# Kernel optimization log

Measured on AMD Instinct MI355X. Metric: run time of the kernel, lower is better.

## Reference

```python
import jax, jax.numpy as jnp
import numpy as np

B, T, N, F, NH, K = 512, 32, 64, 32, 4, 4
D = N * F          # model_dim = 2048
GH = N             # GRU hidden = num_channels
EPS_BN = 1e-5
EPS_LN = 1e-5


def _normalize_A(A):
    # relu -> zero diag -> symmetrize -> sym-normalized Laplacian -> rescale (lmax=2)
    n = A.shape[-1]
    eye = jnp.eye(n, dtype=A.dtype)
    A = jax.nn.relu(A) * (1.0 - eye)
    A = A + A.T
    dinv = 1.0 / jnp.sqrt(jnp.sum(A, axis=1) + 1e-10)
    L = eye - dinv[:, None] * A * dinv[None, :]
    return 2.0 * L / 2.0 - eye


def _cheby(L, k):
    # Chebyshev polynomial basis T_0..T_{k-1} of L, stacked [k, N, N]
    n = L.shape[-1]
    sup = [jnp.eye(n, dtype=L.dtype), L]
    for _ in range(2, k):
        sup.append(2.0 * L @ sup[-1] - sup[-2])
    return jnp.stack(sup[:k])


def _bn(x, g, b, axes):
    # training-mode batch norm (biased variance), stats over `axes`
    m = jnp.mean(x, axes, keepdims=True)
    v = jnp.mean((x - m) ** 2, axes, keepdims=True)
    return (x - m) / jnp.sqrt(v + EPS_BN) * g + b


def _forward(x, A, cheb_W, bn1_g, bn1_b, bn2_g, bn2_b,
             Wq, Wk, Wv, Wf, bf, ln_g, ln_b,
             W_ih, W_hh, b_ih, b_hh, lin_W, lin_b, cls_W, cls_b):
    Bsz, Tn, Nn, Fn = x.shape
    xt = jnp.swapaxes(x, 0, 1)                                   # [T,B,N,F]
    # DGCNN BN1: stats over (B, N) per feature, per time step
    xb = _bn(xt, bn1_g[:, None, None, :], bn1_b[:, None, None, :], (1, 2))
    # per-timestep normalized Laplacian and Chebyshev basis
    Ls = jax.vmap(_normalize_A)(A)                               # [T,N,N]
    cheb = jax.vmap(lambda L: _cheby(L, K))(Ls)                  # [T,K,N,N]
    # Chebynet: sum_k (T_k(L) @ x) @ W_k, then relu
    res = jnp.einsum('tknm,tbmf,tkfo->tbno', cheb, xb, cheb_W)   # [T,B,N,F]
    res = jax.nn.relu(res)
    # per-timestep BatchNorm over flattened (B*N, F)
    y = res.reshape(Tn, Bsz * Nn, Fn)
    y = _bn(y, bn2_g[:, None, :], bn2_b[:, None, :], (1,))
    y = jax.nn.sigmoid(y)                                        # [T,B*N,F]
    # replicate torch's stack/transpose/reshape exactly
    y_seq = jnp.swapaxes(y, 0, 1).reshape(Bsz, Tn, Nn * Fn)      # [B,T,D]
    # multi-head attention (no bias on q/k/v, scale = dh^-0.5)
    dh = D // NH
    def heads(z, W):
        return jnp.swapaxes((z @ W).reshape(Bsz, Tn, NH, dh), 1, 2)  # [B,H,T,dh]
    q, k, v = heads(y_seq, Wq), heads(y_seq, Wk), heads(y_seq, Wv)
    attn = jax.nn.softmax(jnp.einsum('bhqd,bhkd->bhqk', q, k) * dh ** -0.5, axis=-1)
    ctx = jnp.einsum('bhqk,bhkd->bhqd', attn, v)
    ctx = jnp.swapaxes(ctx, 1, 2).reshape(Bsz, Tn, D)
    out = ctx @ Wf + bf
    h = y_seq + out
    mu = jnp.mean(h, -1, keepdims=True)
    var = jnp.mean((h - mu) ** 2, -1, keepdims=True)
    h = (h - mu) / jnp.sqrt(var + EPS_LN) * ln_g + ln_b          # [B,T,D]
    # GRU (torch gate convention), scan over time
    def step(hprev, xt_):
        gi = xt_ @ W_ih.T + b_ih                                  # [B,3H]
        gh = hprev @ W_hh.T + b_hh
        ir, iz, inn = jnp.split(gi, 3, axis=-1)
        hr, hz, hn = jnp.split(gh, 3, axis=-1)
        r = jax.nn.sigmoid(ir + hr)
        zg = jax.nn.sigmoid(iz + hz)
        ng = jnp.tanh(inn + r * hn)
        hnew = (1.0 - zg) * ng + zg * hprev
        return hnew, hnew
    h0 = jnp.zeros((Bsz, GH), x.dtype)
    _, hs = jax.lax.scan(step, h0, jnp.swapaxes(h, 0, 1))        # [T,B,GH]
    y_gru = jax.nn.sigmoid(jnp.swapaxes(hs, 0, 1))               # [B,T,GH]
    out_flat = y_gru.reshape(Bsz, Tn * GH)
    proj = jax.nn.sigmoid(out_flat @ lin_W.T + lin_b)
    proj = proj / jnp.maximum(jnp.linalg.norm(proj, axis=-1, keepdims=True), 1e-12)
    y_pred = jax.nn.sigmoid(out_flat @ cls_W.T + cls_b)
    return proj[:, None, :], y_pred


def setup_inputs() -> dict:
    key = jax.random.key(0)
    ks = jax.random.split(key, 12)
    def nrm(k, shape, s):
        return jax.random.normal(k, shape, dtype=jnp.float32) * s
    return {
        'x': jax.random.normal(ks[0], (B, T, N, F), dtype=jnp.float32),
        'A': jax.random.uniform(ks[1], (T, N, N), minval=0.01, maxval=0.5, dtype=jnp.float32),
        'cheb_W': nrm(ks[2], (T, K, F, F), 0.1),
        'bn1_g': jnp.ones((T, F), jnp.float32), 'bn1_b': jnp.zeros((T, F), jnp.float32),
        'bn2_g': jnp.ones((T, F), jnp.float32), 'bn2_b': jnp.zeros((T, F), jnp.float32),
        'Wq': nrm(ks[3], (D, D), 0.02), 'Wk': nrm(ks[4], (D, D), 0.02), 'Wv': nrm(ks[5], (D, D), 0.02),
        'Wf': nrm(ks[6], (D, D), 0.02), 'bf': jnp.zeros((D,), jnp.float32),
        'ln_g': jnp.ones((D,), jnp.float32), 'ln_b': jnp.zeros((D,), jnp.float32),
        'W_ih': nrm(ks[7], (3 * GH, D), 0.02), 'W_hh': nrm(ks[8], (3 * GH, GH), 0.1),
        'b_ih': jnp.zeros((3 * GH,), jnp.float32), 'b_hh': jnp.zeros((3 * GH,), jnp.float32),
        'lin_W': nrm(ks[9], (128, T * GH), 0.05), 'lin_b': jnp.zeros((128,), jnp.float32),
        'cls_W': nrm(ks[10], (3, T * GH), 0.05), 'cls_b': jnp.zeros((3,), jnp.float32),
    }


def reference(x, A, cheb_W, bn1_g, bn1_b, bn2_g, bn2_b,
              Wq, Wk, Wv, Wf, bf, ln_g, ln_b,
              W_ih, W_hh, b_ih, b_hh, lin_W, lin_b, cls_W, cls_b):
    return _forward(x, A, cheb_W, bn1_g, bn1_b, bn2_g, bn2_b,
                    Wq, Wk, Wv, Wf, bf, ln_g, ln_b,
                    W_ih, W_hh, b_ih, b_hh, lin_W, lin_b, cls_W, cls_b)
```

## Files before the change

kernel.cpp:

```cpp
#include <hip/hip_runtime.h>
#include <hip/hip_bf16.h>

typedef unsigned short u16;
typedef __attribute__((ext_vector_type(8))) short short8;
typedef __attribute__((ext_vector_type(4))) short short4_;
typedef __attribute__((ext_vector_type(4))) float f32x4;

__device__ __forceinline__ u16 f2bf(float f){
  union { float fv; unsigned int u; } v; v.fv = f;
  unsigned int u = v.u;
  u = u + 0x7FFFu + ((u >> 16) & 1u);
  return (u16)(u >> 16);
}
__device__ __forceinline__ float bf2f(u16 h){
  union { unsigned int u; float fv; } v; v.u = ((unsigned int)h) << 16; return v.fv;
}
__device__ __forceinline__ float sigmoidf_(float x){ return 1.f/(1.f + __expf(-x)); }
__device__ __forceinline__ float tanhf_(float x){ return 2.f/(1.f + __expf(-2.f*x)) - 1.f; }

__device__ __forceinline__ void gload16(const void* g, void* l){
  __builtin_amdgcn_global_load_lds(
      (const __attribute__((address_space(1))) void*)g,
      (__attribute__((address_space(3))) void*)l, 16, 0, 0);
}
__device__ __forceinline__ f32x4 mfma_bf16(short8 a, short8 b, f32x4 c){
  return __builtin_amdgcn_mfma_f32_16x16x32_bf16(a, b, c, 0, 0, 0);
}

#define ASM_VMCNT2 asm volatile("s_waitcnt vmcnt(2)" ::: "memory")
#define ASM_VMCNT0 asm volatile("s_waitcnt vmcnt(0)" ::: "memory")
#define ASM_LGK0   asm volatile("s_waitcnt lgkmcnt(0)" ::: "memory")
#define SCHB       __builtin_amdgcn_sched_barrier(0)
#define SBAR       do { asm volatile("" ::: "memory"); __builtin_amdgcn_s_barrier(); asm volatile("" ::: "memory"); } while(0)

constexpr size_t OFF_A    = 0;
constexpr size_t OFF_B    = 67108864;
constexpr size_t OFF_C    = OFF_B + 67108864;
constexpr size_t OFF_D    = OFF_C + 201326592;
constexpr size_t OFF_E    = OFF_D + 67108864;
constexpr size_t OFF_WFT  = OFF_E + 25165824;
constexpr size_t OFF_WIH  = OFF_WFT + 8388608;
constexpr size_t OFF_LHAT = OFF_WIH + 1048576;
constexpr size_t OFF_B1P  = OFF_LHAT + 524288;
constexpr size_t OFF_B1S  = OFF_B1P + 524288;
constexpr size_t OFF_B2P  = OFF_B1S + 8192;
constexpr size_t OFF_B2S  = OFF_B2P + 4194304;
constexpr size_t OFF_TC   = OFF_LHAT;
constexpr size_t OFF_WT2  = OFF_C;
constexpr size_t OFF_GI   = OFF_C;
constexpr size_t OFF_OUTF = OFF_C + 16777216;

__global__ __launch_bounds__(256) void wtrans_kernel(const float* __restrict__ Wq, const float* __restrict__ Wk,
                                                     const float* __restrict__ Wv, const float* __restrict__ Wf,
                                                     u16* __restrict__ WqkvT, u16* __restrict__ WfT)
{
  const int k0 = blockIdx.x*64, n0 = blockIdx.y*64, z = blockIdx.z;
  const float* src = (z==0)?Wq:(z==1)?Wk:(z==2)?Wv:Wf;
  u16* dst = (z<3) ? (WqkvT + (size_t)z*2048*2048) : WfT;
  __shared__ float tile[64][65];
  const int c = threadIdx.x & 63, r0 = threadIdx.x >> 6;
#pragma unroll
  for (int i=0;i<16;++i){ int r = r0 + i*4; tile[r][c] = src[(size_t)(k0+r)*2048 + n0 + c]; }
  __syncthreads();
#pragma unroll
  for (int i=0;i<16;++i){ int r = r0 + i*4; dst[(size_t)(n0+r)*2048 + k0 + c] = f2bf(tile[c][r]); }
}

__global__ __launch_bounds__(256) void wih_kernel(const float* __restrict__ Wih, u16* __restrict__ WT)
{
  const int row = blockIdx.x, tid = threadIdx.x;
#pragma unroll
  for (int i=0;i<8;++i){ int col = tid + i*256;
    float v = (row < 192) ? Wih[(size_t)row*2048 + col] : 0.f;
    WT[(size_t)row*2048 + col] = f2bf(v);
  }
}

__global__ __launch_bounds__(256) void bn1_part_kernel(const float* __restrict__ x, float* __restrict__ part)
{
  const int t = blockIdx.x, sl = blockIdx.y;
  const int f = threadIdx.x & 31, grp = threadIdx.x >> 5;
  float s = 0.f, ss = 0.f;
  for (int bb = 0; bb < 8; ++bb){
    const int b = sl*8 + bb;
    const float* xp = x + ((size_t)(b*32 + t))*2048;
    for (int i = 0; i < 8; ++i){
      int n = i*8 + grp;
      float v = xp[n*32 + f];
      s += v; ss += v*v;
    }
  }
  __shared__ float red[8][32][2];
  red[grp][f][0] = s; red[grp][f][1] = ss;
  __syncthreads();
  if (threadIdx.x < 32){
    float S=0, SS=0;
    for (int g=0; g<8; ++g){ S += red[g][threadIdx.x][0]; SS += red[g][threadIdx.x][1]; }
    size_t o = (((size_t)t*64 + sl)*32 + threadIdx.x)*2;
    part[o] = S; part[o+1] = SS;
  }
}

__global__ __launch_bounds__(256) void bn1_fin_kernel(const float* __restrict__ part, const float* __restrict__ g1,
                                                      const float* __restrict__ b1, float* __restrict__ out)
{
  const int t = blockIdx.x;
  const int f = threadIdx.x & 31, grp = threadIdx.x >> 5;
  float s=0, ss=0;
  for (int sl = grp; sl < 64; sl += 8){
    size_t o = (((size_t)t*64 + sl)*32 + f)*2;
    s += part[o]; ss += part[o+1];
  }
  __shared__ float red[8][32][2];
  red[grp][f][0]=s; red[grp][f][1]=ss;
  __syncthreads();
  if (threadIdx.x < 32){
    float S=0, SS=0;
    for (int g=0; g<8; ++g){ S+=red[g][threadIdx.x][0]; SS+=red[g][threadIdx.x][1]; }
    float mean = S*(1.f/32768.f);
    float var  = SS*(1.f/32768.f) - mean*mean;
    float sc   = g1[t*32+threadIdx.x]*rsqrtf(var + 1e-5f);
    out[(t*32+threadIdx.x)*2]   = sc;
    out[(t*32+threadIdx.x)*2+1] = b1[t*32+threadIdx.x] - mean*sc;
  }
}

__global__ __launch_bounds__(256) void lap2_kernel(const float* __restrict__ A, const float* __restrict__ chebW,
                                                   u16* __restrict__ Tcat, u16* __restrict__ WTg)
{
  const int t = blockIdx.x, tid = threadIdx.x;
  __shared__ float Ar[64][68];
  __shared__ float L1[64][68];
  __shared__ float T2s[64][68];
  __shared__ float dr[64];
#pragma unroll
  for (int i=0;i<16;++i){ int idx = tid + i*256; int r = idx>>6, c = idx&63;
    float v = A[(size_t)t*4096 + idx]; v = fmaxf(v, 0.f); if (r==c) v = 0.f;
    Ar[r][c] = v; }
  __syncthreads();
  if (tid < 64){
    float s = 0;
    for (int c2=0;c2<64;++c2) s += Ar[tid][c2] + Ar[c2][tid];
    dr[tid] = rsqrtf(s + 1e-10f);
  }
  __syncthreads();
#pragma unroll
  for (int i=0;i<16;++i){ int idx = tid + i*256; int r = idx>>6, c = idx&63;
    L1[r][c] = -(Ar[r][c] + Ar[c][r]) * dr[r] * dr[c];
  }
  __syncthreads();
  const int row = tid >> 2, c0 = (tid & 3) << 4;
  float a2[16];
#pragma unroll
  for (int j=0;j<16;++j) a2[j] = 0.f;
#pragma unroll 4
  for (int m=0;m<64;++m){
    float lv = L1[row][m];
#pragma unroll
    for (int j=0;j<16;++j) a2[j] += lv*L1[m][c0+j];
  }
#pragma unroll
  for (int j=0;j<16;++j) T2s[row][c0+j] = 2.f*a2[j] - ((row==c0+j)?1.f:0.f);
  __syncthreads();
  float a3[16];
#pragma unroll
  for (int j=0;j<16;++j) a3[j] = 0.f;
#pragma unroll 4
  for (int m=0;m<64;++m){
    float lv = L1[row][m];
#pragma unroll
    for (int j=0;j<16;++j) a3[j] += lv*T2s[m][c0+j];
  }
  u16* tb = Tcat + (size_t)t*16384 + row*256;
#pragma unroll
  for (int j=0;j<16;++j){
    int c = c0 + j;
    tb[c]       = f2bf((row==c)?1.f:0.f);
    tb[64 + c]  = f2bf(L1[row][c]);
    tb[128 + c] = f2bf(T2s[row][c]);
    tb[192 + c] = f2bf(2.f*a3[j] - L1[row][c]);
  }
#pragma unroll
  for (int i=0;i<16;++i){
    int idx = tid + i*256;
    int k = idx>>10, f = (idx>>5)&31, fo = idx&31;
    WTg[(size_t)t*4096 + k*1024 + fo*32 + f] = f2bf(chebW[(size_t)t*4096 + idx]);
  }
}

__global__ __launch_bounds__(256) void cheby_kernel(const float* __restrict__ x, const u16* __restrict__ Tcat,
                                                    const u16* __restrict__ WTg, const float* __restrict__ bn1ss,
                                                    u16* __restrict__ Rb, float* __restrict__ bn2p)
{
  const int t = blockIdx.x >> 6, grp = blockIdx.x & 63, b0 = grp*8;
  const int tid = threadIdx.x, wid = tid >> 6, lane = tid & 63;
  const int fr = lane & 15, fk = (lane >> 4) << 3;
  const int cc = lane & 15, cr = (lane >> 4) << 2;

  __shared__ u16 Tc[64][264];
  __shared__ u16 Wt[128][40];
  __shared__ u16 Xs[64][40];
  __shared__ u16 Gt[128][72];
  __shared__ float red[4][32][2];
  __shared__ float scs[64];

  if (tid < 64) scs[tid] = bn1ss[t*64 + tid];
  {
    const u16* src = Tcat + (size_t)t*16384;
#pragma unroll
    for (int i=0;i<8;++i){ int idx = tid + i*256; int r = idx>>5, c8 = (idx&31)<<3;
      *(short8*)&Tc[r][c8] = *(const short8*)&src[r*256 + c8]; }
  }
  {
    const u16* src = WTg + (size_t)t*4096;
#pragma unroll
    for (int i=0;i<2;++i){ int idx = tid + i*256; int r = idx>>2, c8 = (idx&3)<<3;
      *(short8*)&Wt[r][c8] = *(const short8*)&src[r*32 + c8]; }
  }
  __syncthreads();

  for (int bb=0; bb<8; ++bb){
    const int b = b0 + bb;
    {
      const float* xr = x + ((size_t)(b*32 + t))*2048;
      f32x4 v0 = *(const f32x4*)&xr[tid*8];
      f32x4 v1 = *(const f32x4*)&xr[tid*8+4];
      const int fb = (tid*8)&31;
      short8 w;
#pragma unroll
      for (int e=0;e<4;++e){
        w[e]   = (short)f2bf(v0[e]*scs[2*(fb+e)]   + scs[2*(fb+e)+1]);
        w[e+4] = (short)f2bf(v1[e]*scs[2*(fb+4+e)] + scs[2*(fb+4+e)+1]);
      }
      *(short8*)&Xs[tid>>2][(tid&3)<<3] = w;
    }
    __syncthreads();
    {
      f32x4 g[4][2] = {};
      short8 xa[4], wb[2];
#pragma unroll
      for (int m2=0;m2<4;++m2) xa[m2] = *(const short8*)&Xs[m2*16 + fr][fk];
#pragma unroll
      for (int j=0;j<2;++j)    wb[j]  = *(const short8*)&Wt[wid*32 + j*16 + fr][fk];
#pragma unroll
      for (int m2=0;m2<4;++m2)
#pragma unroll
        for (int j=0;j<2;++j) g[m2][j] = mfma_bf16(xa[m2], wb[j], g[m2][j]);
#pragma unroll
      for (int m2=0;m2<4;++m2)
#pragma unroll
        for (int j=0;j<2;++j){
          short4_ q;
#pragma unroll
          for (int r=0;r<4;++r) q[r] = (short)f2bf(g[m2][j][r]);
          *(short4_*)&Gt[wid*32 + j*16 + cc][m2*16 + cr] = q;
        }
    }
    __syncthreads();
    f32x4 racc[2] = {};
#pragma unroll
    for (int ks=0; ks<8; ++ks){
      short8 ta  = *(const short8*)&Tc[wid*16 + fr][ks*32 + fk];
      short8 gb0 = *(const short8*)&Gt[(ks>>1)*32 + fr][(ks&1)*32 + fk];
      short8 gb1 = *(const short8*)&Gt[(ks>>1)*32 + 16 + fr][(ks&1)*32 + fk];
      racc[0] = mfma_bf16(ta, gb0, racc[0]);
      racc[1] = mfma_bf16(ta, gb1, racc[1]);
    }
    u16* rrow = Rb + ((size_t)(t*512 + b))*2048;
    float sev[2], sqv[2];
#pragma unroll
    for (int j=0;j<2;++j){
      float s1=0.f, s2=0.f;
#pragma unroll
      for (int r=0;r<4;++r){
        float v = fmaxf(racc[j][r], 0.f);
        rrow[(wid*16 + cr + r)*32 + j*16 + cc] = f2bf(v);
        s1 += v; s2 += v*v;
      }
      sev[j]=s1; sqv[j]=s2;
    }
#pragma unroll
    for (int j=0;j<2;++j){
      sev[j] += __shfl_xor(sev[j], 16, 64); sev[j] += __shfl_xor(sev[j], 32, 64);
      sqv[j] += __shfl_xor(sqv[j], 16, 64); sqv[j] += __shfl_xor(sqv[j], 32, 64);
    }
    if (lane < 16){
#pragma unroll
      for (int j=0;j<2;++j){ red[wid][j*16+cc][0] = sev[j]; red[wid][j*16+cc][1] = sqv[j]; }
    }
    __syncthreads();
    if (tid < 64){
      int f = tid & 31, c = tid >> 5;
      bn2p[((size_t)(t*512+b)*32 + f)*2 + c] = red[0][f][c]+red[1][f][c]+red[2][f][c]+red[3][f][c];
    }
    __syncthreads();
  }
}

__global__ __launch_bounds__(256) void bn2_fin_kernel(const float* __restrict__ part, const float* __restrict__ g2,
                                                      const float* __restrict__ b2, float* __restrict__ out)
{
  const int t = blockIdx.x;
  const int f = threadIdx.x & 31, grp = threadIdx.x >> 5;
  float s=0, ss=0;
  for (int b = grp; b < 512; b += 8){
    size_t o = ((size_t)(t*512+b)*32 + f)*2;
    s += part[o]; ss += part[o+1];
  }
  __shared__ float red[8][32][2];
  red[grp][f][0]=s; red[grp][f][1]=ss;
  __syncthreads();
  if (threadIdx.x < 32){
    float S=0, SS=0;
    for (int g=0; g<8; ++g){ S+=red[g][threadIdx.x][0]; SS+=red[g][threadIdx.x][1]; }
    float mean = S*(1.f/32768.f);
    float var  = SS*(1.f/32768.f) - mean*mean;
    float scv  = g2[t*32+threadIdx.x]*rsqrtf(var + 1e-5f);
    out[(t*32+threadIdx.x)*2]   = scv;
    out[(t*32+threadIdx.x)*2+1] = b2[t*32+threadIdx.x] - mean*scv;
  }
}

__global__ __launch_bounds__(256) void bn2apply_kernel(const u16* __restrict__ Rb, const float* __restrict__ ss,
                                                       u16* __restrict__ YS)
{
  const int t = blockIdx.x >> 9, b = blockIdx.x & 511, tid = threadIdx.x;
  __shared__ float scs[64];
  if (tid < 64) scs[tid] = ss[t*64 + tid];
  __syncthreads();
  const int n = tid >> 2, f0 = (tid & 3) << 3;
  short8 rv = *(const short8*)&Rb[((size_t)(t*512+b))*2048 + tid*8];
  short8 w;
#pragma unroll
  for (int e=0;e<8;++e){
    int f = f0 + e;
    float v = bf2f((u16)rv[e])*scs[f*2] + scs[f*2+1];
    w[e] = (short)f2bf(sigmoidf_(v));
  }
  *(short8*)&YS[((size_t)(b*32 + (n>>1)))*2048 + (n&1)*1024 + t*32 + f0] = w;
}

template<int CB>
__global__ __launch_bounds__(512, 2) void gemm256_kernel(const u16* __restrict__ A, const u16* __restrict__ BT,
                                                         void* __restrict__ C, int M, int N, int K)
{
  __shared__ u16 smem[65536];
  const int tid = threadIdx.x, wid = tid >> 6, lane = tid & 63;
  const int MB = M >> 8, NB = N >> 8;
  const int xcd = (int)blockIdx.x & 7, q = (int)blockIdx.x >> 3;
  const int ppx = NB >> 3;
  const int mb = q / ppx, nb = xcd*ppx + q % ppx;
  (void)MB;
  const int m0 = mb << 8, n0g = nb << 8;
  const int nkt = K >> 6;
  const int nit = nkt >> 1;

  const int wr = wid >> 2, wc = wid & 3;
  const int fr = lane & 15, fk = (lane >> 4) << 3;
  const int cz0 = fk ^ ((fr & 7) << 3);
  const int cz1 = (32 + fk) ^ ((fr & 7) << 3);
  const int srow = wid*16 + (lane >> 3);
  const int scol = ((lane & 7) ^ (lane >> 3)) << 3;
  const int bhalf = wc >> 1, brow0 = (wc & 1) << 6;

  f32x4 acc[8][4] = {};
  short8 af[4][2], bg[4][2];

#define STG(PTR, R0, DSTB, TK, H) do { if ((TK) < nkt) { \
  const u16* _g = (PTR) + (size_t)((R0) + ((H)<<7) + srow)*(size_t)K + (size_t)(((TK)<<6) + scol); \
  u16* _d = &smem[(DSTB) + ((H)<<13) + (wid<<10)]; \
  gload16(_g, _d); gload16(_g + ((size_t)K<<3), _d + 512); } } while(0)

#define DSA(BUF, QM) { _Pragma("unroll") for(int m2=0;m2<4;++m2){ \
  const u16* _p = &smem[(BUF) + wr*8192 + (((QM)*64 + m2*16 + fr)<<6)]; \
  af[m2][0] = *(const short8*)(_p + cz0); af[m2][1] = *(const short8*)(_p + cz1); } }

#define DSB(BUF, QN) { _Pragma("unroll") for(int n2=0;n2<2;++n2){ \
  const u16* _p = &smem[(BUF) + 16384 + bhalf*8192 + ((brow0 + (QN)*32 + n2*16 + fr)<<6)]; \
  bg[(QN)*2+n2][0] = *(const short8*)(_p + cz0); bg[(QN)*2+n2][1] = *(const short8*)(_p + cz1); } }

#define MMA(QM, QN) { __builtin_amdgcn_s_setprio(1); \
  _Pragma("unroll") for(int m2=0;m2<4;++m2) _Pragma("unroll") for(int n2=0;n2<2;++n2) { \
    acc[(QM)*4+m2][(QN)*2+n2] = mfma_bf16(af[m2][0], bg[(QN)*2+n2][0], acc[(QM)*4+m2][(QN)*2+n2]); \
    acc[(QM)*4+m2][(QN)*2+n2] = mfma_bf16(af[m2][1], bg[(QN)*2+n2][1], acc[(QM)*4+m2][(QN)*2+n2]); } \
  __builtin_amdgcn_s_setprio(0); }

  STG(A,  m0,  0,     0, 0); STG(A,  m0,  0,     0, 1);
  STG(BT, n0g, 16384, 0, 0); STG(BT, n0g, 16384, 0, 1);
  STG(A,  m0,  32768, 1, 0);
  ASM_VMCNT2; SBAR;

  for (int i = 0; i < nit; ++i){
    const int kb = i*2;
    DSA(0, 0); DSB(0, 0);
    STG(A, m0, 32768, kb+1, 1);
    SBAR; ASM_LGK0; SCHB; MMA(0,0); SBAR;
    DSB(0, 1);
    STG(BT, n0g, 49152, kb+1, 0);
    SBAR; ASM_LGK0; SCHB; MMA(0,1); SBAR;
    DSA(0, 1);
    STG(BT, n0g, 49152, kb+1, 1);
    SBAR; ASM_LGK0; SCHB; MMA(1,0); SBAR;
    STG(A, m0, 0, kb+2, 0);
    if (kb + 2 >= nkt) { ASM_VMCNT0; } else { ASM_VMCNT2; }
    SBAR; MMA(1,1); SBAR;
    DSA(32768, 0); DSB(32768, 0);
    STG(A, m0, 0, kb+2, 1);
    SBAR; ASM_LGK0; SCHB; MMA(0,0); SBAR;
    DSB(32768, 1);
    STG(BT, n0g, 16384, kb+2, 0);
    SBAR; ASM_LGK0; SCHB; MMA(0,1); SBAR;
    DSA(32768, 1);
    STG(BT, n0g, 16384, kb+2, 1);
    SBAR; ASM_LGK0; SCHB; MMA(1,0); SBAR;
    STG(A, m0, 32768, kb+3, 0);
    ASM_VMCNT2;
    SBAR; MMA(1,1); SBAR;
  }

#undef STG
#undef DSA
#undef DSB
#undef MMA

  const int cr = (lane >> 4) << 2, cc = lane & 15;
#pragma unroll
  for (int mf=0; mf<8; ++mf)
#pragma unroll
    for (int nf=0; nf<4; ++nf)
#pragma unroll
      for (int r=0; r<4; ++r){
        const size_t row = (size_t)(m0 + wr*128 + mf*16 + cr + r);
        const size_t col = (size_t)(n0g + wc*64 + nf*16 + cc);
        if (CB == 0) ((u16*)C)[row*(size_t)N + col] = f2bf(acc[mf][nf][r]);
        else        ((float*)C)[row*(size_t)N + col] = acc[mf][nf][r];
      }
}

template<int CB>
__global__ __launch_bounds__(256) void gemm_bt_kernel(const u16* __restrict__ A, const u16* __restrict__ BT,
                                                      void* __restrict__ C, int M, int N, int K)
{
  __shared__ u16 As[128*32];
  __shared__ u16 Bs[128*32];
  const int tid = threadIdx.x;
  const int wave = tid >> 6, lane = tid & 63;
  const int mblocks = M >> 7;
  const int mb = blockIdx.x % mblocks;
  const int nb = blockIdx.x / mblocks;
  const int lr = lane >> 2;
  const int lc = (lane & 3) << 3;
  const u16* Ag0 = A  + (size_t)(mb*128 + wave*16 + lr)*K + lc;
  const u16* Bg0 = BT + (size_t)(nb*128 + wave*16 + lr)*K + lc;
  const u16* Ag1 = Ag0 + (size_t)64*K;
  const u16* Bg1 = Bg0 + (size_t)64*K;
  u16* lA0 = &As[(wave*16)*32];
  u16* lA1 = &As[(wave*16+64)*32];
  u16* lB0 = &Bs[(wave*16)*32];
  u16* lB1 = &Bs[(wave*16+64)*32];
  const int wm = (wave >> 1)*64, wn = (wave & 1)*64;
  const int fr = lane & 15, fk = (lane >> 4) << 3;
  f32x4 acc[4][4] = {};
  for (int kt = 0; kt < K; kt += 32){
    __syncthreads();
    gload16(Ag0 + kt, lA0);
    gload16(Ag1 + kt, lA1);
    gload16(Bg0 + kt, lB0);
    gload16(Bg1 + kt, lB1);
    __syncthreads();
    short8 af[4], bfr[4];
#pragma unroll
    for (int i=0;i<4;++i) af[i]  = *(const short8*)&As[(wm + i*16 + fr)*32 + fk];
#pragma unroll
    for (int j=0;j<4;++j) bfr[j] = *(const short8*)&Bs[(wn + j*16 + fr)*32 + fk];
#pragma unroll
    for (int i=0;i<4;++i)
#pragma unroll
      for (int j=0;j<4;++j)
        acc[i][j] = mfma_bf16(af[i], bfr[j], acc[i][j]);
  }
  const int cr = (lane >> 4) << 2, cc = lane & 15;
#pragma unroll
  for (int i=0;i<4;++i)
#pragma unroll
    for (int j=0;j<4;++j)
#pragma unroll
      for (int r=0;r<4;++r){
        const size_t row = (size_t)(mb*128 + wm + i*16 + cr + r);
        const size_t col = (size_t)(nb*128 + wn + j*16 + cc);
        if (CB == 0) ((u16*)C)[row*(size_t)N + col] = f2bf(acc[i][j][r]);
        else        ((float*)C)[row*(size_t)N + col] = acc[i][j][r];
      }
}

__global__ __launch_bounds__(256) void attn_kernel(const u16* __restrict__ QKV, u16* __restrict__ CTX)
{
  const int b = blockIdx.x >> 2, h = blockIdx.x & 3;
  const int tid = threadIdx.x;
  const int wave = tid >> 6, lane = tid & 63;
  __shared__ float spart[4][32][33];
  __shared__ float sm[32][33];
  __shared__ float rowinv[32];
  __shared__ u16 pb[32][40];
  __shared__ u16 vt[512][40];

  {
    const int t2 = tid >> 3;
    const size_t vbase = ((size_t)(b*32 + t2))*6144 + 4096 + h*512;
#pragma unroll
    for (int i = 0; i < 8; ++i){
      int d0 = i*64 + (tid & 7)*8;
      short8 v8 = *(const short8*)&QKV[vbase + d0];
#pragma unroll
      for (int e = 0; e < 8; ++e) vt[d0+e][t2] = (u16)v8[e];
    }
  }
  const int fr = lane & 15, fk = (lane >> 4) << 3;
  f32x4 sacc[2][2] = {};
  const size_t qrow = ((size_t)(b*32))*6144 + h*512;
#pragma unroll
  for (int kk = 0; kk < 4; ++kk){
    const int kof = wave*128 + kk*32 + fk;
    short8 qf0 = *(const short8*)&QKV[qrow + (size_t)fr*6144 + kof];
    short8 qf1 = *(const short8*)&QKV[qrow + (size_t)(fr+16)*6144 + kof];
    short8 kf0 = *(const short8*)&QKV[qrow + 2048 + (size_t)fr*6144 + kof];
    short8 kf1 = *(const short8*)&QKV[qrow + 2048 + (size_t)(fr+16)*6144 + kof];
    sacc[0][0] = mfma_bf16(qf0, kf0, sacc[0][0]);
    sacc[0][1] = mfma_bf16(qf0, kf1, sacc[0][1]);
    sacc[1][0] = mfma_bf16(qf1, kf0, sacc[1][0]);
    sacc[1][1] = mfma_bf16(qf1, kf1, sacc[1][1]);
  }
  const int cr = (lane >> 4) << 2, cc = lane & 15;
#pragma unroll
  for (int i=0;i<2;++i)
#pragma unroll
    for (int j=0;j<2;++j)
#pragma unroll
      for (int r=0;r<4;++r) spart[wave][i*16+cr+r][j*16+cc] = sacc[i][j][r];
  __syncthreads();
  const float scl = 0.04419417382415922f;
  for (int e = tid; e < 1024; e += 256){
    int r = e >> 5, c = e & 31;
    sm[r][c] = (spart[0][r][c]+spart[1][r][c]+spart[2][r][c]+spart[3][r][c])*scl;
  }
  __syncthreads();
  if (tid < 32){
    float m = -1e30f;
    for (int c=0;c<32;++c) m = fmaxf(m, sm[tid][c]);
    float s = 0;
    for (int c=0;c<32;++c){ float e = __expf(sm[tid][c]-m); sm[tid][c] = e; s += e; }
    rowinv[tid] = 1.f/s;
  }
  __syncthreads();
  for (int e = tid; e < 1024; e += 256){
    int r = e>>5, c = e&31;
    pb[r][c] = f2bf(sm[r][c]*rowinv[r]);
  }
  __syncthreads();
  f32x4 cacc[2][8] = {};
  short8 pf0 = *(const short8*)&pb[fr][fk];
  short8 pf1 = *(const short8*)&pb[fr+16][fk];
#pragma unroll
  for (int j=0;j<8;++j){
    short8 vf = *(const short8*)&vt[wave*128 + j*16 + fr][fk];
    cacc[0][j] = mfma_bf16(pf0, vf, cacc[0][j]);
    cacc[1][j] = mfma_bf16(pf1, vf, cacc[1][j]);
  }
#pragma unroll
  for (int i=0;i<2;++i)
#pragma unroll
    for (int j=0;j<8;++j)
#pragma unroll
      for (int r=0;r<4;++r){
        int t1 = i*16 + cr + r;
        int d  = wave*128 + j*16 + cc;
        CTX[((size_t)(b*32+t1))*2048 + h*512 + d] = f2bf(cacc[i][j][r]);
      }
}

__global__ __launch_bounds__(256) void ln_kernel(const u16* __restrict__ OUT, const u16* __restrict__ YS,
                                                 const float* __restrict__ bfv, const float* __restrict__ lng,
                                                 const float* __restrict__ lnb, u16* __restrict__ HLN)
{
  const int row = blockIdx.x, tid = threadIdx.x;
  const size_t base = (size_t)row*2048 + tid*8;
  short8 o8 = *(const short8*)&OUT[base];
  short8 y8 = *(const short8*)&YS[base];
  float hv[8]; float s = 0;
#pragma unroll
  for (int e=0;e<8;++e){ float v = bf2f((u16)o8[e]) + bf2f((u16)y8[e]) + bfv[tid*8+e]; hv[e]=v; s += v; }
  __shared__ float red[4];
#pragma unroll
  for (int off=32; off; off>>=1) s += __shfl_down(s, off, 64);
  if ((tid&63)==0) red[tid>>6] = s;
  __syncthreads();
  const float mu = (red[0]+red[1]+red[2]+red[3]) * (1.f/2048.f);
  float s2 = 0;
#pragma unroll
  for (int e=0;e<8;++e){ float d = hv[e]-mu; s2 += d*d; }
  __syncthreads();
#pragma unroll
  for (int off=32; off; off>>=1) s2 += __shfl_down(s2, off, 64);
  if ((tid&63)==0) red[tid>>6] = s2;
  __syncthreads();
  const float rstd = rsqrtf((red[0]+red[1]+red[2]+red[3])*(1.f/2048.f) + 1e-5f);
  short8 w;
#pragma unroll
  for (int e=0;e<8;++e) w[e] = (short)f2bf((hv[e]-mu)*rstd*lng[tid*8+e] + lnb[tid*8+e]);
  *(short8*)&HLN[base] = w;
}

__global__ __launch_bounds__(256) void gru_kernel(const float* __restrict__ GI, const float* __restrict__ Whh,
                                                  const float* __restrict__ bih, const float* __restrict__ bhh,
                                                  float* __restrict__ OUTF)
{
  const int b = blockIdx.x, tid = threadIdx.x;
  __shared__ float w[192*65];
  __shared__ float hprev[64];
  __shared__ float gh[192];
#pragma unroll
  for (int i=0;i<48;++i){ int idx = tid + i*256; w[(idx>>6)*65 + (idx&63)] = Whh[idx]; }
  if (tid < 64) hprev[tid] = 0.f;
  const float bh_ = (tid<192) ? bhh[tid] : 0.f;
  __syncthreads();
  for (int t=0;t<32;++t){
    if (tid < 192){
      float s = bh_;
      const float* wr = &w[tid*65];
#pragma unroll 8
      for (int g=0; g<64; ++g) s += wr[g]*hprev[g];
      gh[tid] = s;
    }
    __syncthreads();
    if (tid < 64){
      const float* gi = GI + ((size_t)(b*32 + t))*256;
      float r  = sigmoidf_(gi[tid]     + bih[tid]     + gh[tid]);
      float z  = sigmoidf_(gi[tid+64]  + bih[tid+64]  + gh[tid+64]);
      float n  = tanhf_(gi[tid+128] + bih[tid+128] + r*gh[tid+128]);
      float hn = (1.f - z)*n + z*hprev[tid];
      hprev[tid] = hn;
      OUTF[(size_t)b*2048 + t*64 + tid] = sigmoidf_(hn);
    }
    __syncthreads();
  }
}

__global__ __launch_bounds__(256) void head_kernel(const float* __restrict__ OUTF, const float* __restrict__ linW,
                                                   const float* __restrict__ linb, const float* __restrict__ clsW,
                                                   const float* __restrict__ clsb, float* __restrict__ outp)
{
  const int b = blockIdx.x, tid = threadIdx.x;
  __shared__ float row[2048];
  __shared__ float pr[128];
  __shared__ float part[256];
  __shared__ float rn;
#pragma unroll
  for (int i=0;i<8;++i) row[tid + i*256] = OUTF[(size_t)b*2048 + tid + i*256];
  __syncthreads();
  {
    const int j = tid & 127, half = tid >> 7;
    const float* wr = linW + (size_t)j*2048 + half*1024;
    const float* xr = &row[half*1024];
    float s = 0;
    for (int k=0;k<1024;++k) s += xr[k]*wr[k];
    part[tid] = s;
  }
  __syncthreads();
  if (tid < 128){
    float v = part[tid] + part[tid+128] + linb[tid];
    v = sigmoidf_(v);
    pr[tid] = v;
    part[tid] = v*v;
  }
  __syncthreads();
  if (tid == 0){
    float ss = 0;
    for (int i2=0;i2<128;++i2) ss += part[i2];
    rn = 1.f/fmaxf(sqrtf(ss), 1e-12f);
  }
  __syncthreads();
  if (tid < 128) outp[(size_t)b*128 + tid] = pr[tid]*rn;
  if (tid < 192){
    const int c = tid >> 6, l = tid & 63;
    const float* wr = clsW + (size_t)c*2048;
    float s = 0;
    for (int k=l; k<2048; k+=64) s += row[k]*wr[k];
#pragma unroll
    for (int off=32; off; off>>=1) s += __shfl_down(s, off, 64);
    if (l == 0) outp[65536 + (size_t)b*3 + c] = sigmoidf_(s + clsb[c]);
  }
}

extern "C" void kernel_launch(void* const* d_in, const int* in_sizes, int n_in,
                              void* d_out, int out_size, void* d_ws, size_t ws_size,
                              hipStream_t stream) {
  const float* x    = (const float*)d_in[0];
  const float* Aadj = (const float*)d_in[1];
  const float* chbW = (const float*)d_in[2];
  const float* bn1g = (const float*)d_in[3];
  const float* bn1b = (const float*)d_in[4];
  const float* bn2g = (const float*)d_in[5];
  const float* bn2b = (const float*)d_in[6];
  const float* Wq   = (const float*)d_in[7];
  const float* Wk   = (const float*)d_in[8];
  const float* Wv   = (const float*)d_in[9];
  const float* Wf   = (const float*)d_in[10];
  const float* bfv  = (const float*)d_in[11];
  const float* lng  = (const float*)d_in[12];
  const float* lnb  = (const float*)d_in[13];
  const float* Wih  = (const float*)d_in[14];
  const float* Whh  = (const float*)d_in[15];
  const float* bih  = (const float*)d_in[16];
  const float* bhh  = (const float*)d_in[17];
  const float* linW = (const float*)d_in[18];
  const float* linb = (const float*)d_in[19];
  const float* clsW = (const float*)d_in[20];
  const float* clsb = (const float*)d_in[21];

  char* ws = (char*)d_ws;
  u16*   Rb    = (u16*)(ws + OFF_A);
  u16*   OUTB  = (u16*)(ws + OFF_A);
  u16*   YSEQ  = (u16*)(ws + OFF_B);
  u16*   QKV   = (u16*)(ws + OFF_C);
  u16*   CTX   = (u16*)(ws + OFF_D);
  u16*   HLN   = (u16*)(ws + OFF_D);
  u16*   WqkvT = (u16*)(ws + OFF_E);
  u16*   WfT   = (u16*)(ws + OFF_WFT);
  u16*   WihT  = (u16*)(ws + OFF_WIH);
  u16*   Tcat  = (u16*)(ws + OFF_TC);
  u16*   WTg   = (u16*)(ws + OFF_WT2);
  float* b1p   = (float*)(ws + OFF_B1P);
  float* b1s   = (float*)(ws + OFF_B1S);
  float* b2p   = (float*)(ws + OFF_B2P);
  float* b2s   = (float*)(ws + OFF_B2S);
  float* GI    = (float*)(ws + OFF_GI);
  float* OUTF  = (float*)(ws + OFF_OUTF);

  wtrans_kernel<<<dim3(32,32,4), 256, 0, stream>>>(Wq, Wk, Wv, Wf, WqkvT, WfT);
  wih_kernel<<<dim3(256), 256, 0, stream>>>(Wih, WihT);
  bn1_part_kernel<<<dim3(32,64), 256, 0, stream>>>(x, b1p);
  bn1_fin_kernel<<<dim3(32), 256, 0, stream>>>(b1p, bn1g, bn1b, b1s);
  lap2_kernel<<<dim3(32), 256, 0, stream>>>(Aadj, chbW, Tcat, WTg);
  cheby_kernel<<<dim3(2048), 256, 0, stream>>>(x, Tcat, WTg, b1s, Rb, b2p);
  bn2_fin_kernel<<<dim3(32), 256, 0, stream>>>(b2p, bn2g, bn2b, b2s);
  bn2apply_kernel<<<dim3(16384), 256, 0, stream>>>(Rb, b2s, YSEQ);
  gemm256_kernel<0><<<dim3(1536), 512, 0, stream>>>(YSEQ, WqkvT, (void*)QKV, 16384, 6144, 2048);
  attn_kernel<<<dim3(2048), 256, 0, stream>>>(QKV, CTX);
  gemm256_kernel<0><<<dim3(512), 512, 0, stream>>>(CTX, WfT, (void*)OUTB, 16384, 2048, 2048);
  ln_kernel<<<dim3(16384), 256, 0, stream>>>(OUTB, YSEQ, bfv, lng, lnb, HLN);
  gemm_bt_kernel<1><<<dim3(256), 256, 0, stream>>>(HLN, WihT, (void*)GI, 16384, 256, 2048);
  gru_kernel<<<dim3(512), 256, 0, stream>>>(GI, Whh, bih, bhh, OUTF);
  head_kernel<<<dim3(512), 256, 0, stream>>>(OUTF, linW, linb, clsW, clsb, (float*)d_out);
}
```

Measured before the change: 946.2 us.

## Software-pipeline LDS fragment reads one step ahead of MFMA in GEMM loop

Double-buffers the A fragments in registers and issues the next LDS fragment reads before the current MFMA block instead of after it. The next iteration's first fragments are prefetched at the end of the loop body. The aim is to hide LDS read latency behind matrix-core work. The cost is extra VGPRs, which may lower occupancy or cause spills, and the ordering of LDS reads against barriers and global-to-LDS stores must stay correct.

```diff
diff --git a/kernel.cpp b/kernel.cpp
--- a/kernel.cpp
+++ b/kernel.cpp
@@ -364,7 +364,7 @@
   const int bhalf = wc >> 1, brow0 = (wc & 1) << 6;
 
   f32x4 acc[8][4] = {};
-  short8 af[4][2], bg[4][2];
+  short8 af[2][4][2], bg[4][2];
 
 #define STG(PTR, R0, DSTB, TK, H) do { if ((TK) < nkt) { \
   const u16* _g = (PTR) + (size_t)((R0) + ((H)<<7) + srow)*(size_t)K + (size_t)(((TK)<<6) + scol); \
@@ -373,7 +373,7 @@
 
 #define DSA(BUF, QM) { _Pragma("unroll") for(int m2=0;m2<4;++m2){ \
   const u16* _p = &smem[(BUF) + wr*8192 + (((QM)*64 + m2*16 + fr)<<6)]; \
-  af[m2][0] = *(const short8*)(_p + cz0); af[m2][1] = *(const short8*)(_p + cz1); } }
+  af[QM][m2][0] = *(const short8*)(_p + cz0); af[QM][m2][1] = *(const short8*)(_p + cz1); } }
 
 #define DSB(BUF, QN) { _Pragma("unroll") for(int n2=0;n2<2;++n2){ \
   const u16* _p = &smem[(BUF) + 16384 + bhalf*8192 + ((brow0 + (QN)*32 + n2*16 + fr)<<6)]; \
@@ -381,41 +381,50 @@
 
 #define MMA(QM, QN) { __builtin_amdgcn_s_setprio(1); \
   _Pragma("unroll") for(int m2=0;m2<4;++m2) _Pragma("unroll") for(int n2=0;n2<2;++n2) { \
-    acc[(QM)*4+m2][(QN)*2+n2] = mfma_bf16(af[m2][0], bg[(QN)*2+n2][0], acc[(QM)*4+m2][(QN)*2+n2]); \
-    acc[(QM)*4+m2][(QN)*2+n2] = mfma_bf16(af[m2][1], bg[(QN)*2+n2][1], acc[(QM)*4+m2][(QN)*2+n2]); } \
+    acc[(QM)*4+m2][(QN)*2+n2] = mfma_bf16(af[QM][m2][0], bg[(QN)*2+n2][0], acc[(QM)*4+m2][(QN)*2+n2]); \
+    acc[(QM)*4+m2][(QN)*2+n2] = mfma_bf16(af[QM][m2][1], bg[(QN)*2+n2][1], acc[(QM)*4+m2][(QN)*2+n2]); } \
   __builtin_amdgcn_s_setprio(0); }
 
   STG(A,  m0,  0,     0, 0); STG(A,  m0,  0,     0, 1);
   STG(BT, n0g, 16384, 0, 0); STG(BT, n0g, 16384, 0, 1);
   STG(A,  m0,  32768, 1, 0);
   ASM_VMCNT2; SBAR;
+  DSA(0, 0); DSB(0, 0);
 
   for (int i = 0; i < nit; ++i){
     const int kb = i*2;
-    DSA(0, 0); DSB(0, 0);
     STG(A, m0, 32768, kb+1, 1);
-    SBAR; ASM_LGK0; SCHB; MMA(0,0); SBAR;
-    DSB(0, 1);
+    SBAR; ASM_LGK0; SCHB;
+    DSB(0, 1); SCHB;
+    MMA(0,0); SBAR;
     STG(BT, n0g, 49152, kb+1, 0);
-    SBAR; ASM_LGK0; SCHB; MMA(0,1); SBAR;
-    DSA(0, 1);
+    SBAR; ASM_LGK0; SCHB;
+    DSA(0, 1); SCHB;
+    MMA(0,1); SBAR;
     STG(BT, n0g, 49152, kb+1, 1);
-    SBAR; ASM_LGK0; SCHB; MMA(1,0); SBAR;
+    SBAR; ASM_LGK0; SCHB;
+    MMA(1,0); SBAR;
     STG(A, m0, 0, kb+2, 0);
     if (kb + 2 >= nkt) { ASM_VMCNT0; } else { ASM_VMCNT2; }
-    SBAR; MMA(1,1); SBAR;
-    DSA(32768, 0); DSB(32768, 0);
+    SBAR; ASM_LGK0; SCHB;
+    DSA(32768, 0); DSB(32768, 0); SCHB;
+    MMA(1,1); SBAR;
     STG(A, m0, 0, kb+2, 1);
-    SBAR; ASM_LGK0; SCHB; MMA(0,0); SBAR;
-    DSB(32768, 1);
+    SBAR; ASM_LGK0; SCHB;
+    DSB(32768, 1); SCHB;
+    MMA(0,0); SBAR;
     STG(BT, n0g, 16384, kb+2, 0);
-    SBAR; ASM_LGK0; SCHB; MMA(0,1); SBAR;
-    DSA(32768, 1);
+    SBAR; ASM_LGK0; SCHB;
+    DSA(32768, 1); SCHB;
+    MMA(0,1); SBAR;
     STG(BT, n0g, 16384, kb+2, 1);
-    SBAR; ASM_LGK0; SCHB; MMA(1,0); SBAR;
+    SBAR; ASM_LGK0; SCHB;
+    MMA(1,0); SBAR;
     STG(A, m0, 32768, kb+3, 0);
     ASM_VMCNT2;
-    SBAR; MMA(1,1); SBAR;
+    SBAR; ASM_LGK0; SCHB;
+    DSA(0, 0); DSB(0, 0); SCHB;
+    MMA(1,1); SBAR;
   }
 
 #undef STG
```

Measured after the change: 1.554 ms. 64.2% more time.
